# Optimization experiments

Measured on AMD Instinct MI355X. Metric: run time of the kernel, lower is better.

The kernel has to match this reference:

```python
import jax, jax.numpy as jnp
import numpy as np

N, S, D = 4, 2048, 1024
H, HD = 16, 64  # heads, head_dim = patch_size // heads
SCALE = 1.0 / np.float32(np.sqrt(D))  # module divides by sqrt(patch_size), not sqrt(head_dim)


def setup_inputs() -> dict:
    key = jax.random.key(0)
    ks = jax.random.split(key, 8)
    return {
        "values": jax.random.normal(ks[0], (N, S, D), dtype=jnp.float32),
        "keys": jax.random.normal(ks[1], (N, S, D), dtype=jnp.float32),
        "query": jax.random.normal(ks[2], (N, S, D), dtype=jnp.float32),
        "Wv": jax.random.normal(ks[3], (HD, HD), dtype=jnp.float32) / np.float32(np.sqrt(HD)),
        "Wk": jax.random.normal(ks[4], (HD, HD), dtype=jnp.float32) / np.float32(np.sqrt(HD)),
        "Wq": jax.random.normal(ks[5], (HD, HD), dtype=jnp.float32) / np.float32(np.sqrt(HD)),
        "Wo": jax.random.normal(ks[6], (D, D), dtype=jnp.float32) / np.float32(np.sqrt(D)),
        "bo": jnp.zeros((D,), dtype=jnp.float32),
    }


def reference(values, keys, query, Wv, Wk, Wq, Wo, bo):
    n, ql = query.shape[0], query.shape[1]
    # reshape to heads, then per-head shared linear projections (torch Linear: x @ W.T)
    v = jnp.einsum('nlhd,ed->nlhe', values.reshape(n, -1, H, HD), Wv)
    k = jnp.einsum('nkhd,ed->nkhe', keys.reshape(n, -1, H, HD), Wk)
    q = jnp.einsum('nqhd,ed->nqhe', query.reshape(n, -1, H, HD), Wq)
    energy = jnp.einsum('nqhd,nkhd->nhqk', q, k)  # [N,H,Sq,Sk]
    attn = jax.nn.softmax(energy * SCALE, axis=3)
    out = jnp.einsum('nhql,nlhd->nqhd', attn, v).reshape(n, ql, H * HD)
    return out @ Wo.T + bo
```

## Files before the change

kernel.cpp:

```cpp
#include <hip/hip_runtime.h>
#include <stdint.h>

typedef _Float16 f16;
typedef f16 half2_t __attribute__((ext_vector_type(2)));
typedef f16 half4_t __attribute__((ext_vector_type(4)));
typedef f16 half8_t __attribute__((ext_vector_type(8)));
typedef __fp16 fp16x2_t __attribute__((ext_vector_type(2)));
typedef float f32x4 __attribute__((ext_vector_type(4)));

#define N_ 4
#define S_ 2048
#define D_ 1024
#define H_ 16
#define HD_ 64
#define LOG2E 1.44269504088896340736f
#define SCALE_ 0.03125f

typedef __attribute__((address_space(1))) void gvoid;
typedef __attribute__((address_space(3))) void lvoid;

__device__ __forceinline__ void load_lds16(const void* g, void* l) {
  __builtin_amdgcn_global_load_lds((gvoid*)(uintptr_t)g, (lvoid*)l, 16, 0, 0);
}

__device__ __forceinline__ f32x4 mfma32(half8_t a, half8_t b, f32x4 c) {
  return __builtin_amdgcn_mfma_f32_16x16x32_f16(a, b, c, 0, 0, 0);
}

__device__ __forceinline__ half2_t pack_f16(float a, float b) {
  fp16x2_t t = __builtin_amdgcn_cvt_pkrtz(a, b);
  return __builtin_bit_cast(half2_t, t);
}

__global__ void wprep(const float* __restrict__ Wv, const float* __restrict__ Wo,
                      const float* __restrict__ Wq, const float* __restrict__ Wk,
                      f16* __restrict__ Wbig, float* __restrict__ Mq) {
  int b = blockIdx.x;
  if (b < 1024) {
    int j = b;
#pragma unroll
    for (int c = 0; c < 4; ++c) {
      int i = c * 256 + threadIdx.x;
      int h = i >> 6, dd = i & 63;
      const float* wo = Wo + (size_t)j * 1024 + h * 64;
      float acc = 0.f;
#pragma unroll 8
      for (int e = 0; e < 64; ++e) acc += Wv[e * 64 + dd] * wo[e];
      Wbig[(size_t)j * 1024 + i] = (f16)acc;
    }
  } else {
    int tid = (b - 1024) * 256 + threadIdx.x;
    int d = tid >> 6, e = tid & 63;
    float acc = 0.f;
#pragma unroll 8
    for (int r = 0; r < 64; ++r) acc += Wq[r * 64 + d] * Wk[r * 64 + e];
    Mq[d * 64 + e] = acc * (SCALE_ * LOG2E);
  }
}

__global__ __launch_bounds__(256) void prep2(const float* __restrict__ Q,
                                             const float* __restrict__ K,
                                             const float* __restrict__ V,
                                             const float* __restrict__ Mq,
                                             f16* __restrict__ q16, f16* __restrict__ k16,
                                             f16* __restrict__ v16) {
  __shared__ char smem[16384];
  int b = blockIdx.x;
  if (b < 512) {
    float* mql = (float*)smem;
#pragma unroll
    for (int c = 0; c < 16; ++c) mql[c * 256 + threadIdx.x] = Mq[c * 256 + threadIdx.x];
    __syncthreads();
    int n = b >> 7, sblk = b & 127;
    int L = threadIdx.x & 63, w = threadIdx.x >> 6;
    int lq = L & 15, hh = w * 4 + (L >> 4);
    int s = sblk * 16 + lq;
    const float* qrow = Q + ((size_t)(n * S_ + s)) * D_ + hh * HD_;
    f32x4 acc4[16];
#pragma unroll
    for (int i = 0; i < 16; ++i) acc4[i] = (f32x4){0.f, 0.f, 0.f, 0.f};
    for (int d4 = 0; d4 < 16; ++d4) {
      f32x4 qv = *(const f32x4*)(qrow + d4 * 4);
#pragma unroll
      for (int dj = 0; dj < 4; ++dj) {
        const f32x4* mrow = (const f32x4*)(mql + (d4 * 4 + dj) * 64);
        float qs = qv[dj];
#pragma unroll
        for (int i = 0; i < 16; ++i) acc4[i] += mrow[i] * qs;
      }
    }
    size_t cbase = ((size_t)((n * 16 + hh) * 128 + sblk)) * 2;
#pragma unroll
    for (int dp = 0; dp < 2; ++dp) {
#pragma unroll
      for (int qd = 0; qd < 4; ++qd) {
        half8_t hv;
        f32x4 a0 = acc4[dp * 8 + qd * 2], a1 = acc4[dp * 8 + qd * 2 + 1];
#pragma unroll
        for (int j = 0; j < 4; ++j) { hv[j] = (f16)a0[j]; hv[4 + j] = (f16)a1[j]; }
        *(half8_t*)(q16 + (cbase + dp) * 512 + (qd * 16 + lq) * 8) = hv;
      }
    }
    const float* krow = K + ((size_t)(n * S_ + s)) * D_ + hh * HD_;
    f32x4 kr[16];
#pragma unroll
    for (int i = 0; i < 16; ++i) kr[i] = *(const f32x4*)(krow + i * 4);
#pragma unroll
    for (int dp = 0; dp < 2; ++dp) {
#pragma unroll
      for (int qd = 0; qd < 4; ++qd) {
        half8_t hv;
        f32x4 a0 = kr[dp * 8 + qd * 2], a1 = kr[dp * 8 + qd * 2 + 1];
#pragma unroll
        for (int j = 0; j < 4; ++j) { hv[j] = (f16)a0[j]; hv[4 + j] = (f16)a1[j]; }
        *(half8_t*)(k16 + (cbase + dp) * 512 + (qd * 16 + lq) * 8) = hv;
      }
    }
  } else {
    f16* lv = (f16*)smem;
    int b2 = b - 512;
    int n = b2 >> 10, hh = (b2 >> 6) & 15, sb = b2 & 63;
    int t = threadIdx.x;
    {
      int r = t >> 3, ic = t & 7;
      const float* src = V + ((size_t)(n * S_ + sb * 32 + r)) * D_ + hh * HD_ + ic * 8;
      f32x4 a = *(const f32x4*)src;
      f32x4 b3 = *(const f32x4*)(src + 4);
      half8_t hv;
#pragma unroll
      for (int j = 0; j < 4; ++j) { hv[j] = (f16)a[j]; hv[4 + j] = (f16)b3[j]; }
      *(half8_t*)(lv + r * 64 + ic * 8) = hv;
    }
    __syncthreads();
    {
      int mt = t >> 6, L = t & 63;
      int quad = L >> 4, ld = L & 15;
      half8_t o;
#pragma unroll
      for (int j = 0; j < 4; ++j) {
        o[j]     = lv[(quad * 4 + j) * 64 + mt * 16 + ld];
        o[4 + j] = lv[(quad * 4 + j + 16) * 64 + mt * 16 + ld];
      }
      *(half8_t*)(v16 + (((size_t)(n * 16 + hh) * 64 + sb) * 4 + mt) * 512 + L * 8) = o;
    }
  }
}

__global__ __launch_bounds__(256, 2) void flash(const f16* __restrict__ q16,
                                                const f16* __restrict__ k16,
                                                const f16* __restrict__ v16,
                                                f16* __restrict__ att) {
  int nh = blockIdx.x;
  int qt = blockIdx.y;
  int L = threadIdx.x & 63, w = threadIdx.x >> 6;
  int lq = L & 15, quad = L >> 4;

  const half8_t* qg = (const half8_t*)q16;
  half8_t qB[4][2];
#pragma unroll
  for (int j = 0; j < 4; ++j) {
    size_t qc = ((size_t)(nh * 128 + qt * 16 + w * 4 + j)) * 2;
    qB[j][0] = qg[qc * 64 + L];
    qB[j][1] = qg[(qc + 1) * 64 + L];
  }

  f32x4 accO[4][4];
#pragma unroll
  for (int j = 0; j < 4; ++j)
#pragma unroll
    for (int i = 0; i < 4; ++i) accO[j][i] = (f32x4){0.f, 0.f, 0.f, 0.f};
  f32x4 lvec[4];
#pragma unroll
  for (int j = 0; j < 4; ++j) lvec[j] = (f32x4){0.f, 0.f, 0.f, 0.f};

  const char* kg = (const char*)k16 + (size_t)nh * 262144 + L * 16;
  const char* vg = (const char*)v16 + (size_t)nh * 262144 + L * 16;

  half8_t kfA[4], vfA[4], pb[4];
  f32x4 aQK[2][4];

#define QK16(KF)                                              \
  {                                                           \
    __builtin_amdgcn_s_setprio(1);                            \
    _Pragma("unroll")                                         \
    for (int u = 0; u < 2; ++u) {                             \
      _Pragma("unroll")                                       \
      for (int j = 0; j < 4; ++j) {                           \
        f32x4 a = (f32x4){0.f, 0.f, 0.f, 0.f};                \
        a = mfma32(KF[u * 2], qB[j][0], a);                   \
        a = mfma32(KF[u * 2 + 1], qB[j][1], a);               \
        aQK[u][j] = a;                                        \
      }                                                       \
    }                                                         \
    __builtin_amdgcn_s_setprio(0);                            \
  }

#define PV16(VF)                                              \
  {                                                           \
    __builtin_amdgcn_s_setprio(1);                            \
    _Pragma("unroll")                                         \
    for (int mt2 = 0; mt2 < 4; ++mt2) {                       \
      _Pragma("unroll")                                       \
      for (int j = 0; j < 4; ++j)                             \
        accO[j][mt2] = mfma32(VF[mt2], pb[j], accO[j][mt2]);  \
    }                                                         \
    __builtin_amdgcn_s_setprio(0);                            \
  }

#define EXPPACK                                                             \
  {                                                                         \
    half4_t pc[2][4];                                                       \
    _Pragma("unroll")                                                       \
    for (int u = 0; u < 2; ++u) {                                           \
      _Pragma("unroll")                                                     \
      for (int j = 0; j < 4; ++j) {                                         \
        f32x4 p;                                                            \
        _Pragma("unroll")                                                   \
        for (int r = 0; r < 4; ++r) p[r] = __builtin_amdgcn_exp2f(aQK[u][j][r]); \
        lvec[j] += p;                                                       \
        pc[u][j] = __builtin_shufflevector(pack_f16(p[0], p[1]),            \
                                           pack_f16(p[2], p[3]), 0, 1, 2, 3); \
      }                                                                     \
    }                                                                       \
    _Pragma("unroll")                                                       \
    for (int j = 0; j < 4; ++j)                                             \
      pb[j] = __builtin_shufflevector(pc[0][j], pc[1][j], 0, 1, 2, 3, 4, 5, 6, 7); \
  }

#pragma unroll
  for (int c = 0; c < 4; ++c) {
    kfA[c] = *(const half8_t*)(kg + c * 1024);
    vfA[c] = *(const half8_t*)(vg + c * 1024);
  }
  QK16(kfA);
#pragma unroll
  for (int c = 0; c < 4; ++c) kfA[c] = *(const half8_t*)(kg + 4096 + c * 1024);
  EXPPACK;

  for (int gg = 1; gg < 64; ++gg) {
    QK16(kfA);
    PV16(vfA);
    if (gg + 1 < 64) {
      const char* kb = kg + (size_t)(gg + 1) * 4096;
#pragma unroll
      for (int c = 0; c < 4; ++c) kfA[c] = *(const half8_t*)(kb + c * 1024);
    }
    {
      const char* vb = vg + (size_t)gg * 4096;
#pragma unroll
      for (int c = 0; c < 4; ++c) vfA[c] = *(const half8_t*)(vb + c * 1024);
    }
    EXPPACK;
  }
  PV16(vfA);

#undef QK16
#undef PV16
#undef EXPPACK

  int n = nh >> 4, h = nh & 15;
#pragma unroll
  for (int j = 0; j < 4; ++j) {
    float l = lvec[j][0] + lvec[j][1] + lvec[j][2] + lvec[j][3];
    l += __shfl_xor(l, 16, 64);
    l += __shfl_xor(l, 32, 64);
    float inv_l = 1.0f / l;
    int s = qt * 256 + w * 64 + j * 16 + lq;
    f16* orow = att + ((size_t)(n * S_ + s)) * D_ + h * HD_;
#pragma unroll
    for (int mt2 = 0; mt2 < 4; ++mt2) {
      half4_t o;
#pragma unroll
      for (int r = 0; r < 4; ++r) o[r] = (f16)(accO[j][mt2][r] * inv_l);
      *(half4_t*)(orow + mt2 * 16 + quad * 4) = o;
    }
  }
}

__global__ __launch_bounds__(256, 2) void ogemm(const f16* __restrict__ A, const f16* __restrict__ Bm,
                                                const float* __restrict__ bias, float* __restrict__ C) {
  __shared__ char lds[32768];
  int bm = blockIdx.x, bn = blockIdx.y;
  int L = threadIdx.x & 63, w = threadIdx.x >> 6;
  int wm = w >> 1, wn = w & 1;
  int lq = L & 15, quad = L >> 4;
  int lr = L >> 2, lc = L & 3;
  int src_c = lc ^ (lr & 3);
  f32x4 acc[16];
#pragma unroll
  for (int i = 0; i < 16; ++i) acc[i] = (f32x4){0.f, 0.f, 0.f, 0.f};

  const f16* ga0 = A + ((size_t)(bm * 128 + (w * 2) * 16 + lr)) * 1024 + src_c * 8;
  const f16* gb0 = Bm + ((size_t)(bn * 128 + (w * 2) * 16 + lr)) * 1024 + src_c * 8;

#pragma unroll
  for (int t = 0; t < 2; ++t)
#pragma unroll
    for (int c = 0; c < 2; ++c) {
      load_lds16(ga0 + t * 32 + (size_t)c * 16 * 1024, lds + t * 16384 + (w * 2 + c) * 1024);
      load_lds16(gb0 + t * 32 + (size_t)c * 16 * 1024, lds + t * 16384 + 8192 + (w * 2 + c) * 1024);
    }
  __syncthreads();

  for (int kt = 0; kt < 32; ++kt) {
    const char* base = lds + (kt & 1) * 16384;
    half8_t af[4], bf[4];
#pragma unroll
    for (int t = 0; t < 4; ++t) {
      int ch = quad ^ (lq & 3);
      af[t] = *(const half8_t*)(base + (wm * 64 + t * 16 + lq) * 64 + ch * 16);
      bf[t] = *(const half8_t*)(base + 8192 + (wn * 64 + t * 16 + lq) * 64 + ch * 16);
    }
#pragma unroll
    for (int mt = 0; mt < 4; ++mt)
#pragma unroll
      for (int nt = 0; nt < 4; ++nt)
        acc[mt * 4 + nt] =
            __builtin_amdgcn_mfma_f32_16x16x32_f16(af[mt], bf[nt], acc[mt * 4 + nt], 0, 0, 0);
    __syncthreads();
    if (kt + 2 < 32) {
      char* dst = lds + (kt & 1) * 16384;
#pragma unroll
      for (int c = 0; c < 2; ++c) {
        load_lds16(ga0 + (kt + 2) * 32 + (size_t)c * 16 * 1024, dst + (w * 2 + c) * 1024);
        load_lds16(gb0 + (kt + 2) * 32 + (size_t)c * 16 * 1024, dst + 8192 + (w * 2 + c) * 1024);
      }
    }
  }

#pragma unroll
  for (int nt = 0; nt < 4; ++nt) {
    int col = bn * 128 + wn * 64 + nt * 16 + lq;
    float bv = bias[col];
#pragma unroll
    for (int mt = 0; mt < 4; ++mt) {
#pragma unroll
      for (int r = 0; r < 4; ++r) {
        int row = bm * 128 + wm * 64 + mt * 16 + quad * 4 + r;
        C[(size_t)row * 1024 + col] = acc[mt * 4 + nt][r] + bv;
      }
    }
  }
}

extern "C" void kernel_launch(void* const* d_in, const int* in_sizes, int n_in,
                              void* d_out, int out_size, void* d_ws, size_t ws_size,
                              hipStream_t stream) {
  const float* V  = (const float*)d_in[0];
  const float* K  = (const float*)d_in[1];
  const float* Q  = (const float*)d_in[2];
  const float* Wv = (const float*)d_in[3];
  const float* Wk = (const float*)d_in[4];
  const float* Wq = (const float*)d_in[5];
  const float* Wo = (const float*)d_in[6];
  const float* bo = (const float*)d_in[7];
  float* out = (float*)d_out;

  char* ws = (char*)d_ws;
  float* Mq  = (float*)(ws);
  f16* Wbig  = (f16*)(ws + (1ull << 20));
  f16* q16   = (f16*)(ws + (3ull << 20));
  f16* k16   = (f16*)(ws + (19ull << 20));
  f16* v16   = (f16*)(ws + (35ull << 20));
  f16* att   = (f16*)(ws + (51ull << 20));

  wprep<<<1040, 256, 0, stream>>>(Wv, Wo, Wq, Wk, Wbig, Mq);
  prep2<<<4608, 256, 0, stream>>>(Q, K, V, Mq, q16, k16, v16);
  flash<<<dim3(64, 8), 256, 0, stream>>>(q16, k16, v16, att);
  ogemm<<<dim3(64, 8), 256, 0, stream>>>(att, Wbig, bo, out);
}
```

Baseline: 269.5 us.

## Split Q/K prep into LDS-staged kernel and fold V conversion into wprep

The V fp16 transpose work moves into the weight-prep kernel, so it runs alongside the Wbig/Mq computation. Q/K preparation gets its own kernel that stages Q rows and Mq in LDS using async global-to-LDS loads with an XOR swizzle. Each block covers half the heads, and K is converted with coalesced row loads. This aims to fix the uncoalesced per-lane strided Q/K global reads and overlap the V work with weight prep. It uses more LDS per block and also raises the ogemm occupancy hint to 3.

Measured after the change: 263.0 us. 2.4% less time.

```diff
diff --git a/kernel.cpp b/kernel.cpp
--- a/kernel.cpp
+++ b/kernel.cpp
@@ -34,7 +34,10 @@
 
 __global__ void wprep(const float* __restrict__ Wv, const float* __restrict__ Wo,
                       const float* __restrict__ Wq, const float* __restrict__ Wk,
-                      f16* __restrict__ Wbig, float* __restrict__ Mq) {
+                      const float* __restrict__ V,
+                      f16* __restrict__ Wbig, float* __restrict__ Mq,
+                      f16* __restrict__ v16) {
+  __shared__ char smem[16384];
   int b = blockIdx.x;
   if (b < 1024) {
     int j = b;
@@ -48,77 +51,16 @@
       for (int e = 0; e < 64; ++e) acc += Wv[e * 64 + dd] * wo[e];
       Wbig[(size_t)j * 1024 + i] = (f16)acc;
     }
-  } else {
+  } else if (b < 1040) {
     int tid = (b - 1024) * 256 + threadIdx.x;
     int d = tid >> 6, e = tid & 63;
     float acc = 0.f;
 #pragma unroll 8
     for (int r = 0; r < 64; ++r) acc += Wq[r * 64 + d] * Wk[r * 64 + e];
     Mq[d * 64 + e] = acc * (SCALE_ * LOG2E);
-  }
-}
-
-__global__ __launch_bounds__(256) void prep2(const float* __restrict__ Q,
-                                             const float* __restrict__ K,
-                                             const float* __restrict__ V,
-                                             const float* __restrict__ Mq,
-                                             f16* __restrict__ q16, f16* __restrict__ k16,
-                                             f16* __restrict__ v16) {
-  __shared__ char smem[16384];
-  int b = blockIdx.x;
-  if (b < 512) {
-    float* mql = (float*)smem;
-#pragma unroll
-    for (int c = 0; c < 16; ++c) mql[c * 256 + threadIdx.x] = Mq[c * 256 + threadIdx.x];
-    __syncthreads();
-    int n = b >> 7, sblk = b & 127;
-    int L = threadIdx.x & 63, w = threadIdx.x >> 6;
-    int lq = L & 15, hh = w * 4 + (L >> 4);
-    int s = sblk * 16 + lq;
-    const float* qrow = Q + ((size_t)(n * S_ + s)) * D_ + hh * HD_;
-    f32x4 acc4[16];
-#pragma unroll
-    for (int i = 0; i < 16; ++i) acc4[i] = (f32x4){0.f, 0.f, 0.f, 0.f};
-    for (int d4 = 0; d4 < 16; ++d4) {
-      f32x4 qv = *(const f32x4*)(qrow + d4 * 4);
-#pragma unroll
-      for (int dj = 0; dj < 4; ++dj) {
-        const f32x4* mrow = (const f32x4*)(mql + (d4 * 4 + dj) * 64);
-        float qs = qv[dj];
-#pragma unroll
-        for (int i = 0; i < 16; ++i) acc4[i] += mrow[i] * qs;
-      }
-    }
-    size_t cbase = ((size_t)((n * 16 + hh) * 128 + sblk)) * 2;
-#pragma unroll
-    for (int dp = 0; dp < 2; ++dp) {
-#pragma unroll
-      for (int qd = 0; qd < 4; ++qd) {
-        half8_t hv;
-        f32x4 a0 = acc4[dp * 8 + qd * 2], a1 = acc4[dp * 8 + qd * 2 + 1];
-#pragma unroll
-        for (int j = 0; j < 4; ++j) { hv[j] = (f16)a0[j]; hv[4 + j] = (f16)a1[j]; }
-        *(half8_t*)(q16 + (cbase + dp) * 512 + (qd * 16 + lq) * 8) = hv;
-      }
-    }
-    const float* krow = K + ((size_t)(n * S_ + s)) * D_ + hh * HD_;
-    f32x4 kr[16];
-#pragma unroll
-    for (int i = 0; i < 16; ++i) kr[i] = *(const f32x4*)(krow + i * 4);
-#pragma unroll
-    for (int dp = 0; dp < 2; ++dp) {
-#pragma unroll
-      for (int qd = 0; qd < 4; ++qd) {
-        half8_t hv;
-        f32x4 a0 = kr[dp * 8 + qd * 2], a1 = kr[dp * 8 + qd * 2 + 1];
-#pragma unroll
-        for (int j = 0; j < 4; ++j) { hv[j] = (f16)a0[j]; hv[4 + j] = (f16)a1[j]; }
-        *(half8_t*)(k16 + (cbase + dp) * 512 + (qd * 16 + lq) * 8) = hv;
-      }
-    }
   } else {
     f16* lv = (f16*)smem;
-    int b2 = b - 512;
+    int b2 = b - 1040;
     int n = b2 >> 10, hh = (b2 >> 6) & 15, sb = b2 & 63;
     int t = threadIdx.x;
     {
@@ -143,6 +85,76 @@
       }
       *(half8_t*)(v16 + (((size_t)(n * 16 + hh) * 64 + sb) * 4 + mt) * 512 + L * 8) = o;
     }
+  }
+}
+
+__global__ __launch_bounds__(256, 3) void prep_qk(const float* __restrict__ Q,
+                                                  const float* __restrict__ K,
+                                                  const float* __restrict__ Mq,
+                                                  f16* __restrict__ q16,
+                                                  f16* __restrict__ k16) {
+  __shared__ char smem[49152];
+  int b = blockIdx.x;
+  int hhalf = b & 1;
+  int sblk = (b >> 1) & 127;
+  int n = b >> 8;
+  int t = threadIdx.x;
+  int L = t & 63, w = t >> 6;
+
+  const char* Qblk = (const char*)(Q + ((size_t)(n * S_ + sblk * 16)) * D_) + hhalf * 2048;
+#pragma unroll
+  for (int i = 0; i < 8; ++i) {
+    int g = (w * 8 + i) * 64 + L;
+    int row = g >> 7, hhg = (g >> 4) & 7, sl = g & 15;
+    load_lds16(Qblk + (size_t)row * 4096 + hhg * 256 + ((sl ^ (row & 7)) << 4),
+               smem + (w * 8 + i) * 1024);
+  }
+#pragma unroll
+  for (int j = 0; j < 4; ++j)
+    load_lds16((const char*)Mq + (size_t)(((w * 4 + j) * 64 + L) << 4),
+               smem + 32768 + (w * 4 + j) * 1024);
+
+  const char* Kblk = (const char*)(K + ((size_t)(n * S_ + sblk * 16)) * D_) + hhalf * 2048;
+#pragma unroll
+  for (int i = 0; i < 4; ++i) {
+    int e = i * 256 + t;
+    int r = e >> 6, c6 = e & 63;
+    const char* src = Kblk + (size_t)r * 4096 + c6 * 32;
+    f32x4 a = *(const f32x4*)src;
+    f32x4 b2 = *(const f32x4*)(src + 16);
+    half8_t hv;
+#pragma unroll
+    for (int jj = 0; jj < 4; ++jj) { hv[jj] = (f16)a[jj]; hv[4 + jj] = (f16)b2[jj]; }
+    int hk = hhalf * 8 + (c6 >> 3), cc = c6 & 7, dp = cc >> 2, qd = cc & 3;
+    *(half8_t*)(k16 + ((((size_t)(n * 16 + hk) * 128 + sblk) * 2 + dp) * 512) +
+                (qd * 16 + r) * 8) = hv;
+  }
+  __syncthreads();
+
+  int lq = t & 15, hh8 = (t >> 4) & 7, eh = t >> 7;
+  int head = hhalf * 8 + hh8;
+  const float* mql = (const float*)(smem + 32768);
+  f32x4 acc4[8];
+#pragma unroll
+  for (int i = 0; i < 8; ++i) acc4[i] = (f32x4){0.f, 0.f, 0.f, 0.f};
+  for (int d4 = 0; d4 < 16; ++d4) {
+    f32x4 qv = *(const f32x4*)(smem + lq * 2048 + hh8 * 256 + ((d4 ^ (lq & 7)) << 4));
+#pragma unroll
+    for (int dj = 0; dj < 4; ++dj) {
+      const f32x4* mrow = (const f32x4*)(mql + (d4 * 4 + dj) * 64 + eh * 32);
+      float qs = qv[dj];
+#pragma unroll
+      for (int i = 0; i < 8; ++i) acc4[i] += mrow[i] * qs;
+    }
+  }
+  size_t cbase = ((size_t)((n * 16 + head) * 128 + sblk)) * 2;
+#pragma unroll
+  for (int qd = 0; qd < 4; ++qd) {
+    half8_t hv;
+    f32x4 a0 = acc4[qd * 2], a1 = acc4[qd * 2 + 1];
+#pragma unroll
+    for (int jj = 0; jj < 4; ++jj) { hv[jj] = (f16)a0[jj]; hv[4 + jj] = (f16)a1[jj]; }
+    *(half8_t*)(q16 + (cbase + eh) * 512 + (qd * 16 + lq) * 8) = hv;
   }
 }
 
@@ -277,7 +289,7 @@
   }
 }
 
-__global__ __launch_bounds__(256, 2) void ogemm(const f16* __restrict__ A, const f16* __restrict__ Bm,
+__global__ __launch_bounds__(256, 3) void ogemm(const f16* __restrict__ A, const f16* __restrict__ Bm,
                                                 const float* __restrict__ bias, float* __restrict__ C) {
   __shared__ char lds[32768];
   int bm = blockIdx.x, bn = blockIdx.y;
@@ -364,8 +376,8 @@
   f16* v16   = (f16*)(ws + (35ull << 20));
   f16* att   = (f16*)(ws + (51ull << 20));
 
-  wprep<<<1040, 256, 0, stream>>>(Wv, Wo, Wq, Wk, Wbig, Mq);
-  prep2<<<4608, 256, 0, stream>>>(Q, K, V, Mq, q16, k16, v16);
+  wprep<<<5136, 256, 0, stream>>>(Wv, Wo, Wq, Wk, V, Wbig, Mq, v16);
+  prep_qk<<<1024, 256, 0, stream>>>(Q, K, Mq, q16, k16);
   flash<<<dim3(64, 8), 256, 0, stream>>>(q16, k16, v16, att);
   ogemm<<<dim3(64, 8), 256, 0, stream>>>(att, Wbig, bo, out);
 }
```
